# Kernel tuning notes

Measured on AMD Instinct MI355X. Metric: run time of the kernel, lower is better.

Reference implementation:

```python
import jax, jax.numpy as jnp
import numpy as np

EMB_LEN = 1024
HEAD_SIZE = 64

def setup_inputs() -> dict:
    key = jax.random.key(0)
    k1, k2, k3, k4 = jax.random.split(key, 4)
    input_emb = jax.random.normal(k1, (8, 4096, EMB_LEN), dtype=jnp.float32)
    # nn.Linear weights are [out, in]; applied as x @ W.T
    Wq = jax.random.normal(k2, (HEAD_SIZE, EMB_LEN), dtype=jnp.float32) * (EMB_LEN ** -0.5)
    Wk = jax.random.normal(k3, (HEAD_SIZE, EMB_LEN), dtype=jnp.float32) * (EMB_LEN ** -0.5)
    Wv = jax.random.normal(k4, (HEAD_SIZE, EMB_LEN), dtype=jnp.float32) * (EMB_LEN ** -0.5)
    return {"input_emb": input_emb, "Wq": Wq, "Wk": Wk, "Wv": Wv}

def reference(input_emb, Wq, Wk, Wv):
    B, S, E = input_emb.shape
    scale = jnp.asarray(HEAD_SIZE, input_emb.dtype) ** -0.5
    q = jnp.einsum('bse,he->bsh', input_emb, Wq)  # [B,S,H]
    k = jnp.einsum('bse,he->bsh', input_emb, Wk)
    v = jnp.einsum('bse,he->bsh', input_emb, Wv)
    scores = jnp.einsum('bqh,bkh->bqk', q, k) * scale  # [B,S,S]
    causal = jnp.tril(jnp.ones((S, S), dtype=bool))
    scores = jnp.where(causal, scores, -jnp.inf)
    attn = jax.nn.softmax(scores, axis=-1)
    return jnp.einsum('bqk,bkh->bqh', attn, v)
```

## Files before the change

### kernel.cpp

```cpp
#include <hip/hip_runtime.h>
#include <hip/hip_bf16.h>

#define EMB 1024
#define HS 64
#define SEQ 4096

using bf16x8 = __attribute__((ext_vector_type(8))) __bf16;
using f32x4  = __attribute__((ext_vector_type(4))) float;
using f32x16 = __attribute__((ext_vector_type(16))) float;

__device__ __forceinline__ ushort f2b(float f) {
    unsigned x = __float_as_uint(f);
    return (ushort)((x + 0x7fffu + ((x >> 16) & 1u)) >> 16);
}

__global__ void cvt_w(const float* __restrict__ wq, const float* __restrict__ wk,
                      const float* __restrict__ wv, ushort* __restrict__ wcat) {
    int i = blockIdx.x * 256 + threadIdx.x;
    const int n = HS * EMB;
    if (i >= 3 * n) return;
    float f;
    if (i < n)          f = wq[i];
    else if (i < 2 * n) f = wk[i - n];
    else                f = wv[i - 2 * n];
    wcat[i] = f2b(f);
}

__global__ __launch_bounds__(1024) void qkv_proj(
        const float* __restrict__ x, const ushort* __restrict__ wcat,
        ushort* __restrict__ qo, ushort* __restrict__ ko, ushort* __restrict__ vo) {
    __shared__ ushort Xs[64][72];
    __shared__ ushort Ws[192][72];
    const int t = threadIdx.x;
    const int lane = t & 63, wid = t >> 6;
    const int g = lane >> 4, c = lane & 15;
    const int strip = wid >> 2, colq = wid & 3;
    const int row0 = blockIdx.x * 64;

    f32x4 acc[3];
#pragma unroll
    for (int i = 0; i < 3; ++i) acc[i] = f32x4{0.f, 0.f, 0.f, 0.f};

    for (int kc = 0; kc < EMB; kc += 64) {
        __syncthreads();
        {
            int e = t * 4, r = e >> 6, cc = e & 63;
            float4 v = *reinterpret_cast<const float4*>(&x[(row0 + r) * EMB + kc + cc]);
            ushort4 u;
            u.x = f2b(v.x); u.y = f2b(v.y); u.z = f2b(v.z); u.w = f2b(v.w);
            *reinterpret_cast<ushort4*>(&Xs[r][cc]) = u;
        }
#pragma unroll
        for (int i = 0; i < 3; ++i) {
            int e = (i * 1024 + t) * 4, r = e >> 6, cc = e & 63;
            *reinterpret_cast<ushort4*>(&Ws[r][cc]) =
                *reinterpret_cast<const ushort4*>(&wcat[r * EMB + kc + cc]);
        }
        __syncthreads();
#pragma unroll
        for (int kk = 0; kk < 2; ++kk) {
            bf16x8 a = *reinterpret_cast<const bf16x8*>(&Xs[strip * 16 + c][kk * 32 + 8 * g]);
#pragma unroll
            for (int nt = 0; nt < 3; ++nt) {
                bf16x8 b = *reinterpret_cast<const bf16x8*>(
                    &Ws[(colq * 3 + nt) * 16 + c][kk * 32 + 8 * g]);
                acc[nt] = __builtin_amdgcn_mfma_f32_16x16x32_bf16(a, b, acc[nt], 0, 0, 0);
            }
        }
    }

    const float qs = 0.125f * 1.44269504f;
#pragma unroll
    for (int nt = 0; nt < 3; ++nt) {
        int col = (colq * 3 + nt) * 16 + c;
        int rowb = row0 + strip * 16 + 4 * g;
        if (col < 64) {
#pragma unroll
            for (int r = 0; r < 4; ++r)
                qo[(rowb + r) * 64 + col] = f2b(acc[nt][r] * qs);
        } else if (col < 128) {
#pragma unroll
            for (int r = 0; r < 4; ++r)
                ko[(rowb + r) * 64 + (col - 64)] = f2b(acc[nt][r]);
        } else {
            int b = rowb >> 12, s0 = rowb & 4095;
            ushort4 pv;
            pv.x = f2b(acc[nt][0]); pv.y = f2b(acc[nt][1]);
            pv.z = f2b(acc[nt][2]); pv.w = f2b(acc[nt][3]);
            *reinterpret_cast<ushort4*>(&vo[(b * 64 + (col - 128)) * SEQ + s0]) = pv;
        }
    }
}

__global__ __launch_bounds__(256) void attn(
        const ushort* __restrict__ q, const ushort* __restrict__ k,
        const ushort* __restrict__ vt, float* __restrict__ out, float* __restrict__ L) {
    __shared__ __align__(16) char smem[32768];

    const int t = threadIdx.x;
    const int lane = t & 63, w = t >> 6;
    const int ql = lane & 31, h = lane >> 5;

    const int batch = blockIdx.x & 7;
    const int x = 143 - (int)(blockIdx.x >> 3);
    int gi = 0;
#pragma unroll
    for (int g2 = 1; g2 <= 7; ++g2) if (x >= 2 * g2 * (g2 + 1)) gi = g2;
    const int off = x - 2 * gi * (gi + 1);
    const int ns = gi + 1;
    const int j = off / ns;
    const int seg = off - j * ns;
    const int qt = 4 * gi + j;
    const int T = 2 * (qt + 1);
    const int Td = T / ns, Tr = T % ns;
    const int t0 = seg * Td + (seg < Tr ? seg : Tr);
    const int tcnt = Td + (seg < Tr ? 1 : 0);

    const int q0w = qt * 128 + w * 32;

    const ushort* qb = q + (size_t)batch * SEQ * 64;
    const ushort* kb = k + (size_t)batch * SEQ * 64;
    const ushort* vb = vt + (size_t)batch * 64 * SEQ;

    bf16x8 qa[4];
#pragma unroll
    for (int ks = 0; ks < 4; ++ks)
        qa[ks] = *reinterpret_cast<const bf16x8*>(&qb[(q0w + ql) * 64 + ks * 16 + 8 * h]);

    f32x16 accO0, accO1;
#pragma unroll
    for (int r = 0; r < 16; ++r) { accO0[r] = 0.f; accO1[r] = 0.f; }
    float lsum = 0.f;

    auto stage = [&](int tile, int buf) {
        const int kv0 = tile * 64;
#pragma unroll
        for (int n = 0; n < 4; ++n) {
            const int fid = w * 4 + n;
            const ushort* src;
            if (fid < 8)
                src = &kb[(size_t)(kv0 + (fid >> 2) * 32 + ql) * 64 + (fid & 3) * 16 + 8 * h];
            else
                src = &vb[(size_t)(((fid - 8) >> 2) * 32 + ql) * SEQ + kv0 + ((fid - 8) & 3) * 16 + 8 * h];
            char* dst = smem + buf * 16384 + fid * 1024 + lane * 16;
            __builtin_amdgcn_global_load_lds(
                (const __attribute__((address_space(1))) void*)src,
                (__attribute__((address_space(3))) void*)dst, 16, 0, 0);
        }
    };

    stage(t0, 0);

    for (int ti = 0; ti < tcnt; ++ti) {
        asm volatile("s_waitcnt vmcnt(0)" ::: "memory");
        __builtin_amdgcn_s_barrier();
        __builtin_amdgcn_sched_barrier(0);
        if (ti + 1 < tcnt) stage(t0 + ti + 1, (ti + 1) & 1);

        const char* kbase = smem + (ti & 1) * 16384;
        const char* vbase = kbase + 8192;
        const int kv0 = (t0 + ti) * 64;
        const bool cross = (kv0 + 64 > q0w);

#pragma unroll
        for (int kt2 = 0; kt2 < 2; ++kt2) {
            f32x16 S;
#pragma unroll
            for (int r = 0; r < 16; ++r) S[r] = 0.f;
#pragma unroll
            for (int ks = 0; ks < 4; ++ks) {
                bf16x8 kf = *reinterpret_cast<const bf16x8*>(kbase + (kt2 * 4 + ks) * 1024 + lane * 16);
                S = __builtin_amdgcn_mfma_f32_32x32x16_bf16(kf, qa[ks], S, 0, 0, 0);
            }
            if (cross) {
#pragma unroll
                for (int r = 0; r < 16; ++r) {
                    int kv = kv0 + kt2 * 32 + (r & 3) + 8 * (r >> 2) + 4 * h;
                    if (kv > q0w + ql) S[r] = -INFINITY;
                }
            }
            uint d0, d1, d2, d3, d4, d5, d6, d7;
            {
                float p[16];
#pragma unroll
                for (int r = 0; r < 16; ++r) {
                    p[r] = __builtin_amdgcn_exp2f(S[r]);
                    lsum += p[r];
                }
                asm("v_cvt_pk_bf16_f32 %0, %1, %2" : "=v"(d0) : "v"(p[0]),  "v"(p[1]));
                asm("v_cvt_pk_bf16_f32 %0, %1, %2" : "=v"(d1) : "v"(p[2]),  "v"(p[3]));
                asm("v_cvt_pk_bf16_f32 %0, %1, %2" : "=v"(d2) : "v"(p[4]),  "v"(p[5]));
                asm("v_cvt_pk_bf16_f32 %0, %1, %2" : "=v"(d3) : "v"(p[6]),  "v"(p[7]));
                asm("v_cvt_pk_bf16_f32 %0, %1, %2" : "=v"(d4) : "v"(p[8]),  "v"(p[9]));
                asm("v_cvt_pk_bf16_f32 %0, %1, %2" : "=v"(d5) : "v"(p[10]), "v"(p[11]));
                asm("v_cvt_pk_bf16_f32 %0, %1, %2" : "=v"(d6) : "v"(p[12]), "v"(p[13]));
                asm("v_cvt_pk_bf16_f32 %0, %1, %2" : "=v"(d7) : "v"(p[14]), "v"(p[15]));
            }
#pragma unroll
            for (int kk = 0; kk < 2; ++kk) {
                uint a0 = kk ? d4 : d0, a1 = kk ? d5 : d1;
                uint b0 = kk ? d6 : d2, b1 = kk ? d7 : d3;
                asm("v_permlane32_swap_b32 %0, %1" : "+v"(a0), "+v"(b0));
                asm("v_permlane32_swap_b32 %0, %1" : "+v"(a1), "+v"(b1));
                uint pw[4] = {a0, a1, b0, b1};
                bf16x8 pa = *reinterpret_cast<bf16x8*>(pw);
                const int kk2 = kt2 * 2 + kk;
                bf16x8 vf0 = *reinterpret_cast<const bf16x8*>(vbase + (0 * 4 + kk2) * 1024 + lane * 16);
                bf16x8 vf1 = *reinterpret_cast<const bf16x8*>(vbase + (1 * 4 + kk2) * 1024 + lane * 16);
                accO0 = __builtin_amdgcn_mfma_f32_32x32x16_bf16(pa, vf0, accO0, 0, 0, 0);
                accO1 = __builtin_amdgcn_mfma_f32_32x32x16_bf16(pa, vf1, accO1, 0, 0, 0);
            }
        }
    }

    lsum += __shfl_xor(lsum, 32, 64);
    float* ob = out + (size_t)batch * SEQ * 64;
#pragma unroll
    for (int r = 0; r < 16; ++r) {
        int qrow = q0w + (r & 3) + 8 * (r >> 2) + 4 * h;
        atomicAdd(&ob[(size_t)qrow * 64 + ql], accO0[r]);
        atomicAdd(&ob[(size_t)qrow * 64 + 32 + ql], accO1[r]);
    }
    if (h == 0) atomicAdd(&L[batch * SEQ + q0w + ql], lsum);
}

__global__ __launch_bounds__(256) void norm_out(float* __restrict__ out,
                                                const float* __restrict__ L) {
    int i = blockIdx.x * 256 + threadIdx.x;
    float4 v = reinterpret_cast<float4*>(out)[i];
    float inv = 1.0f / L[i >> 4];
    v.x *= inv; v.y *= inv; v.z *= inv; v.w *= inv;
    reinterpret_cast<float4*>(out)[i] = v;
}

extern "C" void kernel_launch(void* const* d_in, const int* in_sizes, int n_in,
                              void* d_out, int out_size, void* d_ws, size_t ws_size,
                              hipStream_t stream) {
    const float* x  = (const float*)d_in[0];
    const float* wq = (const float*)d_in[1];
    const float* wk = (const float*)d_in[2];
    const float* wv = (const float*)d_in[3];
    float* out = (float*)d_out;

    char* ws = (char*)d_ws;
    ushort* wcat = (ushort*)ws;
    ushort* qo   = (ushort*)(ws + 393216);
    ushort* ko   = (ushort*)(ws + 393216 + 4194304);
    ushort* vo   = (ushort*)(ws + 393216 + 2 * 4194304);
    float*  Lb   = (float*)(ws + 393216 + 3 * 4194304);

    hipMemsetAsync(out, 0, (size_t)8 * SEQ * 64 * 4, stream);
    hipMemsetAsync(Lb, 0, (size_t)8 * SEQ * 4, stream);
    hipLaunchKernelGGL(cvt_w, dim3(768), dim3(256), 0, stream, wq, wk, wv, wcat);
    hipLaunchKernelGGL(qkv_proj, dim3(512), dim3(1024), 0, stream, x, wcat, qo, ko, vo);
    hipLaunchKernelGGL(attn, dim3(1152), dim3(256), 0, stream, qo, ko, vo, out, Lb);
    hipLaunchKernelGGL(norm_out, dim3(2048), dim3(256), 0, stream, out, Lb);
}
```

Baseline: 94.56 us.

## Use 512-thread attention blocks over 256-row query tiles with fixed 4-tile KV segments

Restructures the attention work split. Each block now covers a 256-row query tile with 8 waves and a fixed segment of 4 KV tiles, using a triangular index mapping instead of the old variable-length segment scheme. Tiles entirely above the diagonal are skipped per wave. The two QK^T MFMA chains are interleaved, and MFMA sections are wrapped in s_setprio, aiming to share each K/V tile load across more waves and improve MFMA issue. Risks include idle waves on diagonal tiles, more barrier contention in bigger blocks, and more atomics per output row.

```diff
diff --git a/kernel.cpp b/kernel.cpp
--- a/kernel.cpp
+++ b/kernel.cpp
@@ -92,7 +92,7 @@
     }
 }
 
-__global__ __launch_bounds__(256) void attn(
+__global__ __launch_bounds__(512) void attn(
         const ushort* __restrict__ q, const ushort* __restrict__ k,
         const ushort* __restrict__ vt, float* __restrict__ out, float* __restrict__ L) {
     __shared__ __align__(16) char smem[32768];
@@ -102,21 +102,13 @@
     const int ql = lane & 31, h = lane >> 5;
 
     const int batch = blockIdx.x & 7;
-    const int x = 143 - (int)(blockIdx.x >> 3);
-    int gi = 0;
-#pragma unroll
-    for (int g2 = 1; g2 <= 7; ++g2) if (x >= 2 * g2 * (g2 + 1)) gi = g2;
-    const int off = x - 2 * gi * (gi + 1);
-    const int ns = gi + 1;
-    const int j = off / ns;
-    const int seg = off - j * ns;
-    const int qt = 4 * gi + j;
-    const int T = 2 * (qt + 1);
-    const int Td = T / ns, Tr = T % ns;
-    const int t0 = seg * Td + (seg < Tr ? seg : Tr);
-    const int tcnt = Td + (seg < Tr ? 1 : 0);
-
-    const int q0w = qt * 128 + w * 32;
+    const int s = (int)(blockIdx.x >> 3);
+    int qt = 0;
+#pragma unroll
+    for (int qq = 1; qq < 16; ++qq) if (s >= (qq * (qq + 1)) >> 1) qt = qq;
+    const int seg = s - ((qt * (qt + 1)) >> 1);
+    const int t0 = seg * 4;
+    const int q0w = qt * 256 + w * 32;
 
     const ushort* qb = q + (size_t)batch * SEQ * 64;
     const ushort* kb = k + (size_t)batch * SEQ * 64;
@@ -135,8 +127,8 @@
     auto stage = [&](int tile, int buf) {
         const int kv0 = tile * 64;
 #pragma unroll
-        for (int n = 0; n < 4; ++n) {
-            const int fid = w * 4 + n;
+        for (int n = 0; n < 2; ++n) {
+            const int fid = w * 2 + n;
             const ushort* src;
             if (fid < 8)
                 src = &kb[(size_t)(kv0 + (fid >> 2) * 32 + ql) * 64 + (fid & 3) * 16 + 8 * h];
@@ -151,64 +143,69 @@
 
     stage(t0, 0);
 
-    for (int ti = 0; ti < tcnt; ++ti) {
+    for (int ti = 0; ti < 4; ++ti) {
         asm volatile("s_waitcnt vmcnt(0)" ::: "memory");
         __builtin_amdgcn_s_barrier();
         __builtin_amdgcn_sched_barrier(0);
-        if (ti + 1 < tcnt) stage(t0 + ti + 1, (ti + 1) & 1);
+        if (ti + 1 < 4) stage(t0 + ti + 1, (ti + 1) & 1);
 
         const char* kbase = smem + (ti & 1) * 16384;
         const char* vbase = kbase + 8192;
         const int kv0 = (t0 + ti) * 64;
+        if (kv0 >= q0w + 32) continue;
         const bool cross = (kv0 + 64 > q0w);
 
+        f32x16 S0, S1;
+#pragma unroll
+        for (int r = 0; r < 16; ++r) { S0[r] = 0.f; S1[r] = 0.f; }
+        __builtin_amdgcn_s_setprio(1);
+#pragma unroll
+        for (int ks = 0; ks < 4; ++ks) {
+            bf16x8 kf0 = *reinterpret_cast<const bf16x8*>(kbase + ks * 1024 + lane * 16);
+            bf16x8 kf1 = *reinterpret_cast<const bf16x8*>(kbase + (4 + ks) * 1024 + lane * 16);
+            S0 = __builtin_amdgcn_mfma_f32_32x32x16_bf16(kf0, qa[ks], S0, 0, 0, 0);
+            S1 = __builtin_amdgcn_mfma_f32_32x32x16_bf16(kf1, qa[ks], S1, 0, 0, 0);
+        }
+        __builtin_amdgcn_s_setprio(0);
+
+        if (cross) {
+#pragma unroll
+            for (int r = 0; r < 16; ++r) {
+                int kvr = kv0 + (r & 3) + 8 * (r >> 2) + 4 * h;
+                if (kvr > q0w + ql)      S0[r] = -INFINITY;
+                if (kvr + 32 > q0w + ql) S1[r] = -INFINITY;
+            }
+        }
+
+        uint d[2][8];
+#pragma unroll
+        for (int i = 0; i < 8; ++i) {
+            float a0 = __builtin_amdgcn_exp2f(S0[2 * i]);
+            float a1 = __builtin_amdgcn_exp2f(S0[2 * i + 1]);
+            float b0 = __builtin_amdgcn_exp2f(S1[2 * i]);
+            float b1 = __builtin_amdgcn_exp2f(S1[2 * i + 1]);
+            lsum += (a0 + a1) + (b0 + b1);
+            asm("v_cvt_pk_bf16_f32 %0, %1, %2" : "=v"(d[0][i]) : "v"(a0), "v"(a1));
+            asm("v_cvt_pk_bf16_f32 %0, %1, %2" : "=v"(d[1][i]) : "v"(b0), "v"(b1));
+        }
+
 #pragma unroll
         for (int kt2 = 0; kt2 < 2; ++kt2) {
-            f32x16 S;
-#pragma unroll
-            for (int r = 0; r < 16; ++r) S[r] = 0.f;
-#pragma unroll
-            for (int ks = 0; ks < 4; ++ks) {
-                bf16x8 kf = *reinterpret_cast<const bf16x8*>(kbase + (kt2 * 4 + ks) * 1024 + lane * 16);
-                S = __builtin_amdgcn_mfma_f32_32x32x16_bf16(kf, qa[ks], S, 0, 0, 0);
-            }
-            if (cross) {
-#pragma unroll
-                for (int r = 0; r < 16; ++r) {
-                    int kv = kv0 + kt2 * 32 + (r & 3) + 8 * (r >> 2) + 4 * h;
-                    if (kv > q0w + ql) S[r] = -INFINITY;
-                }
-            }
-            uint d0, d1, d2, d3, d4, d5, d6, d7;
-            {
-                float p[16];
-#pragma unroll
-                for (int r = 0; r < 16; ++r) {
-                    p[r] = __builtin_amdgcn_exp2f(S[r]);
-                    lsum += p[r];
-                }
-                asm("v_cvt_pk_bf16_f32 %0, %1, %2" : "=v"(d0) : "v"(p[0]),  "v"(p[1]));
-                asm("v_cvt_pk_bf16_f32 %0, %1, %2" : "=v"(d1) : "v"(p[2]),  "v"(p[3]));
-                asm("v_cvt_pk_bf16_f32 %0, %1, %2" : "=v"(d2) : "v"(p[4]),  "v"(p[5]));
-                asm("v_cvt_pk_bf16_f32 %0, %1, %2" : "=v"(d3) : "v"(p[6]),  "v"(p[7]));
-                asm("v_cvt_pk_bf16_f32 %0, %1, %2" : "=v"(d4) : "v"(p[8]),  "v"(p[9]));
-                asm("v_cvt_pk_bf16_f32 %0, %1, %2" : "=v"(d5) : "v"(p[10]), "v"(p[11]));
-                asm("v_cvt_pk_bf16_f32 %0, %1, %2" : "=v"(d6) : "v"(p[12]), "v"(p[13]));
-                asm("v_cvt_pk_bf16_f32 %0, %1, %2" : "=v"(d7) : "v"(p[14]), "v"(p[15]));
-            }
 #pragma unroll
             for (int kk = 0; kk < 2; ++kk) {
-                uint a0 = kk ? d4 : d0, a1 = kk ? d5 : d1;
-                uint b0 = kk ? d6 : d2, b1 = kk ? d7 : d3;
+                uint a0 = d[kt2][kk * 4 + 0], a1 = d[kt2][kk * 4 + 1];
+                uint b0 = d[kt2][kk * 4 + 2], b1 = d[kt2][kk * 4 + 3];
                 asm("v_permlane32_swap_b32 %0, %1" : "+v"(a0), "+v"(b0));
                 asm("v_permlane32_swap_b32 %0, %1" : "+v"(a1), "+v"(b1));
                 uint pw[4] = {a0, a1, b0, b1};
                 bf16x8 pa = *reinterpret_cast<bf16x8*>(pw);
                 const int kk2 = kt2 * 2 + kk;
-                bf16x8 vf0 = *reinterpret_cast<const bf16x8*>(vbase + (0 * 4 + kk2) * 1024 + lane * 16);
-                bf16x8 vf1 = *reinterpret_cast<const bf16x8*>(vbase + (1 * 4 + kk2) * 1024 + lane * 16);
+                bf16x8 vf0 = *reinterpret_cast<const bf16x8*>(vbase + kk2 * 1024 + lane * 16);
+                bf16x8 vf1 = *reinterpret_cast<const bf16x8*>(vbase + (4 + kk2) * 1024 + lane * 16);
+                __builtin_amdgcn_s_setprio(1);
                 accO0 = __builtin_amdgcn_mfma_f32_32x32x16_bf16(pa, vf0, accO0, 0, 0, 0);
                 accO1 = __builtin_amdgcn_mfma_f32_32x32x16_bf16(pa, vf1, accO1, 0, 0, 0);
+                __builtin_amdgcn_s_setprio(0);
             }
         }
     }
@@ -253,6 +250,6 @@
     hipMemsetAsync(Lb, 0, (size_t)8 * SEQ * 4, stream);
     hipLaunchKernelGGL(cvt_w, dim3(768), dim3(256), 0, stream, wq, wk, wv, wcat);
     hipLaunchKernelGGL(qkv_proj, dim3(512), dim3(1024), 0, stream, x, wcat, qo, ko, vo);
-    hipLaunchKernelGGL(attn, dim3(1152), dim3(256), 0, stream, qo, ko, vo, out, Lb);
+    hipLaunchKernelGGL(attn, dim3(1088), dim3(512), 0, stream, qo, ko, vo, out, Lb);
     hipLaunchKernelGGL(norm_out, dim3(2048), dim3(256), 0, stream, out, Lb);
 }
```

Measured after the change: 113.4 us. +19.9%, slower.
